# Performance work log

Hardware: AMD Instinct MI355X
Metric: run time of the kernel (lower is better)

## Reference

```python
import jax, jax.numpy as jnp
import numpy as np

A = 256          # image height (x_shape[0])
B = 256          # image width  (x_shape[1])
N = 64           # filterbank grid size
H_DIM = 1024     # hidden dim
BATCH = 512
MAX_DIM = max(A, B)


def _compute_F(params):
    """Build NxA and NxB Gaussian filterbank matrices from 5 attention params.
    Faithful to the torch code: .item() calls on g_X, g_Y, d cut gradients,
    replicated here with stop_gradient; global (not row-wise) normalization;
    var = exp(params[2] + 1e-8) as in the source."""
    gt_X, gt_Y = params[0], params[1]
    var = jnp.exp(params[2] + 1e-8)
    dt = jnp.exp(params[3])
    g_X = jax.lax.stop_gradient((A + 1) * (gt_X + 1) / 2)
    g_Y = jax.lax.stop_gradient((B + 1) * (gt_Y + 1) / 2)
    d = jax.lax.stop_gradient(dt * (MAX_DIM - 1) / (N - 1))
    sub_val = (-N * 0.5 - 0.5) * d  # first linspace endpoint offset; step == d
    idx = jnp.arange(N, dtype=params.dtype)
    mu_X = g_X + sub_val + d * idx  # == linspace(g_X+sub, g_X+add, N)
    mu_Y = g_Y + sub_val + d * idx
    a = jnp.arange(A, dtype=params.dtype)
    b = jnp.arange(B, dtype=params.dtype)
    F_X = jnp.exp(-(a[None, :] - mu_X[:, None]) ** 2 / (2 * var))  # [N, A]
    F_Y = jnp.exp(-(b[None, :] - mu_Y[:, None]) ** 2 / (2 * var))  # [N, B]
    F_X = F_X / jnp.sum(F_X)
    F_Y = F_Y / jnp.sum(F_Y)
    return F_X, F_Y


def setup_inputs() -> dict:
    key = jax.random.key(0)
    k1, k2, k3, k4, k5 = jax.random.split(key, 5)
    x = jax.random.uniform(k1, (BATCH, A * B), dtype=jnp.float32)
    x_hat = jax.random.normal(k2, (BATCH, A * B), dtype=jnp.float32)
    h = jax.random.normal(k3, (BATCH, H_DIM), dtype=jnp.float32)
    # small init scale keeps exp(params) in a sane range
    W_read_w = jax.random.normal(k4, (5, H_DIM), dtype=jnp.float32) * 0.02
    W_read_b = jax.random.normal(k5, (5,), dtype=jnp.float32) * 0.01
    return {"x": x, "x_hat": x_hat, "h": h, "W_read_w": W_read_w, "W_read_b": W_read_b}


def reference(x, x_hat, h, W_read_w, W_read_b):
    # params from the FIRST batch element only, as in the torch code ([0])
    params = (h @ W_read_w.T + W_read_b)[0]  # [5]
    gamma = jnp.exp(params[4])
    F_X, F_Y = _compute_F(params)
    xi = x.reshape(-1, A, B)
    xh = x_hat.reshape(-1, A, B)

    def filt(im):
        # gamma * F_Y @ im @ F_X^T : [x, N, N]
        return gamma * jnp.einsum('na,xab,mb->xnm', F_Y, im, F_X)

    x_filt = filt(xi).reshape(-1, N * N)
    x_hat_filt = filt(xh).reshape(-1, N * N)
    return jnp.concatenate([x_filt, x_hat_filt], axis=1)  # [batch, 2*N^2]
```

## Files before the change

kernel.cpp:

```cpp
#include <hip/hip_runtime.h>
#include <math.h>

#define N_FILT 64
#define IMG_DIM 256
#define IMG_SZ (256*256)
#define HDIM 1024
#define NBATCH 512


__global__ __launch_bounds__(256) void k_prep(
    const float* __restrict__ h, const float* __restrict__ Ww,
    const float* __restrict__ Wb, int* __restrict__ meta,
    float* __restrict__ fyg, float* __restrict__ fxg)
{
  __shared__ float partial[32];
  __shared__ float par_s[8];
  __shared__ float F[N_FILT*IMG_DIM];
  __shared__ int s_lo[64], s_hi[64], s_glo[16], s_ghi[16];
  __shared__ float ssum[4];
  const int t   = threadIdx.x;
  const int side= blockIdx.x;
  const int wv  = t>>6, ln = t&63;
  float* __restrict__ wout = side ? fxg : fyg;

  {
    float4 z = make_float4(0.f,0.f,0.f,0.f);
    float4* p = (float4*)wout;
    #pragma unroll
    for (int k=0;k<16;++k) p[t + 256*k] = z;
  }

  {
    float s0=0.f,s1=0.f,s2=0.f,s3=0.f,s4=0.f;
    for (int k=t;k<HDIM;k+=256){
      const float hv=h[k];
      s0=fmaf(hv,Ww[k        ],s0);
      s1=fmaf(hv,Ww[HDIM+k   ],s1);
      s2=fmaf(hv,Ww[2*HDIM+k ],s2);
      s3=fmaf(hv,Ww[3*HDIM+k ],s3);
      s4=fmaf(hv,Ww[4*HDIM+k ],s4);
    }
    #pragma unroll
    for (int o=32;o>0;o>>=1){
      s0+=__shfl_down(s0,o); s1+=__shfl_down(s1,o); s2+=__shfl_down(s2,o);
      s3+=__shfl_down(s3,o); s4+=__shfl_down(s4,o);
    }
    if (ln==0){ partial[wv*8+0]=s0; partial[wv*8+1]=s1; partial[wv*8+2]=s2;
                partial[wv*8+3]=s3; partial[wv*8+4]=s4; }
  }
  __syncthreads();
  if (t<5) par_s[t]=partial[t]+partial[8+t]+partial[16+t]+partial[24+t]+Wb[t];
  __syncthreads();

  const float var   = expf(par_s[2]+1e-8f);
  const float dt    = expf(par_s[3]);
  const float gamma = expf(par_s[4]);
  const float gC = 0.5f*257.f*(par_s[side?0:1]+1.f);
  const float d  = dt*(255.f/63.f);
  const float sub= -32.5f*d;
  const float inv2v = 1.f/(2.f*var);
  const float w88v  = 88.f*var;

  if (t<64){
    float mu = gC + sub + d*(float)t;
    float astar = fminf(255.f, fmaxf(0.f, rintf(mu)));
    float t0 = (astar-mu)*(astar-mu);
    float r  = sqrtf(t0 + w88v);
    int lo = (int)ceilf(mu-r); int hi = (int)floorf(mu+r)+1;
    lo = lo<0?0:lo; hi = hi>256?256:hi; if (hi<lo) hi=lo;
    s_lo[t]=lo; s_hi[t]=hi;
  }
  __syncthreads();
  if (t<16){
    int lo=256, hi=0;
    #pragma unroll
    for (int k2=0;k2<4;++k2){ lo=min(lo,s_lo[t*4+k2]); hi=max(hi,s_hi[t*4+k2]); }
    if (hi<lo){lo=0;hi=0;}
    if (side==0){ meta[t]=lo; meta[16+t]=hi; }
    else        { lo &= ~3;  meta[32+t]=lo; meta[48+t]=hi; }
    s_glo[t]=lo; s_ghi[t]=hi;
  }
  float sum=0.f;
  #pragma unroll
  for (int k=0;k<64;++k){
    int idx=t+256*k;
    int n=idx>>8, a=idx&255;
    float mu = gC+sub+d*(float)n;
    float dx=(float)a-mu;
    float e=expf(-dx*dx*inv2v);
    F[idx]=e; sum+=e;
  }
  #pragma unroll
  for (int o=32;o>0;o>>=1) sum+=__shfl_down(sum,o);
  if (ln==0) ssum[wv]=sum;
  __syncthreads();
  const float stot = ssum[0]+ssum[1]+ssum[2]+ssum[3];
  const float sc = (side==0 ? gamma : 1.f)/stot;
  #pragma unroll
  for (int k=0;k<64;++k){
    int idx=t+256*k;
    int n=idx>>8, a=idx&255, g=n>>2;
    int lo=s_glo[g], hi=s_ghi[g];
    if (a>=lo && a<hi) wout[(size_t)((g<<10)+((a-lo)<<2)+(n&3))] = F[idx]*sc;
  }
}

__global__ __launch_bounds__(256, 5) void k_main(
    const float* __restrict__ x, const float* __restrict__ xh,
    const int* __restrict__ meta, const float* __restrict__ fyg,
    const float* __restrict__ fxg, float* __restrict__ out)
{
  __shared__ float Tt[16*256];
  const int bid = blockIdx.x;
  const int lg  = ((bid&7)<<9) | (bid>>3);
  const int img = lg>>2, qq = lg&3;
  const int tid = threadIdx.x;
  const int w    = __builtin_amdgcn_readfirstlane(tid>>6);
  const int lane = tid & 63;
  const float* __restrict__ src = (img<NBATCH) ? (x  + (size_t)img*IMG_SZ)
                                               : (xh + (size_t)(img-NBATCH)*IMG_SZ);
  float* __restrict__ dst = ((img<NBATCH) ? (out + (size_t)img*8192)
                                          : (out + (size_t)(img-NBATCH)*8192 + 4096))
                            + qq*1024;

  {
    const int g  = qq*4 + w;
    const int a0 = __builtin_amdgcn_readfirstlane(meta[g]);
    const int nr = __builtin_amdgcn_readfirstlane(meta[16+g]) - a0;
    const int C  = (nr + 7) >> 3;
    const float* rp0 = src + 4*lane;
    const float* wp  = fyg + ((size_t)g<<10);
    float acc[4][4];
    #pragma unroll
    for (int k2=0;k2<4;++k2){acc[k2][0]=0.f;acc[k2][1]=0.f;acc[k2][2]=0.f;acc[k2][3]=0.f;}
    #pragma unroll 1
    for (int c=0; c<C; ++c){
      float4 A[8];
      float wt0[8], wt1[8], wt2[8], wt3[8];
      #pragma unroll
      for (int j=0;j<8;++j){
        int ra = a0 + c*8 + j; ra = ra>255?255:ra;
        A[j] = *(const float4* __restrict__)(rp0 + (ra<<8));
        int rw = c*8 + j; rw = rw>255?255:rw;
        const float* wr = wp + (rw<<2);
        wt0[j]=wr[0]; wt1[j]=wr[1]; wt2[j]=wr[2]; wt3[j]=wr[3];
      }
      __builtin_amdgcn_sched_barrier(0);
      #pragma unroll
      for (int j=0;j<8;++j){
        acc[0][0]=fmaf(wt0[j],A[j].x,acc[0][0]); acc[0][1]=fmaf(wt0[j],A[j].y,acc[0][1]);
        acc[0][2]=fmaf(wt0[j],A[j].z,acc[0][2]); acc[0][3]=fmaf(wt0[j],A[j].w,acc[0][3]);
        acc[1][0]=fmaf(wt1[j],A[j].x,acc[1][0]); acc[1][1]=fmaf(wt1[j],A[j].y,acc[1][1]);
        acc[1][2]=fmaf(wt1[j],A[j].z,acc[1][2]); acc[1][3]=fmaf(wt1[j],A[j].w,acc[1][3]);
        acc[2][0]=fmaf(wt2[j],A[j].x,acc[2][0]); acc[2][1]=fmaf(wt2[j],A[j].y,acc[2][1]);
        acc[2][2]=fmaf(wt2[j],A[j].z,acc[2][2]); acc[2][3]=fmaf(wt2[j],A[j].w,acc[2][3]);
        acc[3][0]=fmaf(wt3[j],A[j].x,acc[3][0]); acc[3][1]=fmaf(wt3[j],A[j].y,acc[3][1]);
        acc[3][2]=fmaf(wt3[j],A[j].z,acc[3][2]); acc[3][3]=fmaf(wt3[j],A[j].w,acc[3][3]);
      }
      __builtin_amdgcn_sched_barrier(0);
    }
    #pragma unroll
    for (int k2=0;k2<4;++k2){
      const int n = w*4 + k2;
      float4 v; v.x=acc[k2][0]; v.y=acc[k2][1]; v.z=acc[k2][2]; v.w=acc[k2][3];
      *(float4*)&Tt[(n<<8) + ((lane ^ n)<<2)] = v;
    }
  }
  __syncthreads();

  const int nl = lane & 15;
  const int cc = lane >> 4;
  const int q  = w*4 + cc;
  const int lo4 = meta[32+q];
  const int hi  = meta[48+q];
  int ngu = (hi - lo4 + 3) >> 2;
  ngu = max(ngu, __shfl_xor(ngu,16));
  ngu = max(ngu, __shfl_xor(ngu,32));
  const int u0  = lo4 >> 2;
  const float* wq = fxg + ((size_t)q<<10);
  float o0=0.f,o1=0.f,o2=0.f,o3=0.f;
  #pragma unroll 1
  for (int it=0; it<ngu; it+=2){
    const int uA = min(u0+it,   63);
    const int uB = min(u0+it+1, 63);
    const float4 tvA = *(const float4*)&Tt[(nl<<8) + ((uA ^ nl)<<2)];
    const float4 tvB = *(const float4*)&Tt[(nl<<8) + ((uB ^ nl)<<2)];
    const float4 a0w = *(const float4*)(wq + it*16);
    const float4 a1w = *(const float4*)(wq + it*16 + 4);
    const float4 a2w = *(const float4*)(wq + it*16 + 8);
    const float4 a3w = *(const float4*)(wq + it*16 + 12);
    const float4 b0w = *(const float4*)(wq + it*16 + 16);
    const float4 b1w = *(const float4*)(wq + it*16 + 20);
    const float4 b2w = *(const float4*)(wq + it*16 + 24);
    const float4 b3w = *(const float4*)(wq + it*16 + 28);
    __builtin_amdgcn_sched_barrier(0);
    o0=fmaf(tvA.x,a0w.x,fmaf(tvA.y,a1w.x,fmaf(tvA.z,a2w.x,fmaf(tvA.w,a3w.x,o0))));
    o1=fmaf(tvA.x,a0w.y,fmaf(tvA.y,a1w.y,fmaf(tvA.z,a2w.y,fmaf(tvA.w,a3w.y,o1))));
    o2=fmaf(tvA.x,a0w.z,fmaf(tvA.y,a1w.z,fmaf(tvA.z,a2w.z,fmaf(tvA.w,a3w.z,o2))));
    o3=fmaf(tvA.x,a0w.w,fmaf(tvA.y,a1w.w,fmaf(tvA.z,a2w.w,fmaf(tvA.w,a3w.w,o3))));
    if (it+1 < ngu){
      o0=fmaf(tvB.x,b0w.x,fmaf(tvB.y,b1w.x,fmaf(tvB.z,b2w.x,fmaf(tvB.w,b3w.x,o0))));
      o1=fmaf(tvB.x,b0w.y,fmaf(tvB.y,b1w.y,fmaf(tvB.z,b2w.y,fmaf(tvB.w,b3w.y,o1))));
      o2=fmaf(tvB.x,b0w.z,fmaf(tvB.y,b1w.z,fmaf(tvB.z,b2w.z,fmaf(tvB.w,b3w.z,o2))));
      o3=fmaf(tvB.x,b0w.w,fmaf(tvB.y,b1w.w,fmaf(tvB.z,b2w.w,fmaf(tvB.w,b3w.w,o3))));
    }
    __builtin_amdgcn_sched_barrier(0);
  }
  __syncthreads();

  {
    const int m0 = q*4;
    Tt[nl*68 + m0 + 0] = o0; Tt[nl*68 + m0 + 1] = o1;
    Tt[nl*68 + m0 + 2] = o2; Tt[nl*68 + m0 + 3] = o3;
  }
  __syncthreads();
  {
    const int f = tid*4;
    const int n = f>>6, m = f&63;
    const float4 v = *(const float4*)&Tt[n*68+m];
    *(float4*)(dst+f) = v;
  }
}

extern "C" void kernel_launch(void* const* d_in, const int* in_sizes, int n_in,
                              void* d_out, int out_size, void* d_ws, size_t ws_size,
                              hipStream_t stream)
{
  const float* x  = (const float*)d_in[0];
  const float* xh = (const float*)d_in[1];
  const float* h  = (const float*)d_in[2];
  const float* Ww = (const float*)d_in[3];
  const float* Wb = (const float*)d_in[4];
  float* out = (float*)d_out;

  int*   meta = (int*)d_ws;
  float* fyg  = (float*)((char*)d_ws + 256);
  float* fxg  = (float*)((char*)d_ws + 256 + 65536);

  k_prep<<<2, 256, 0, stream>>>(h, Ww, Wb, meta, fyg, fxg);
  k_main<<<8*NBATCH, 256, 0, stream>>>(x, xh, meta, fyg, fxg, out);
}
```

Before: 96.63 us.

## Stream image rows into LDS with double-buffered async global_load_lds

```diff
diff --git a/kernel.cpp b/kernel.cpp
--- a/kernel.cpp
+++ b/kernel.cpp
@@ -7,6 +7,13 @@
 #define HDIM 1024
 #define NBATCH 512
 
+
+__device__ __forceinline__ void gl_lds16(const float* g, float* l){
+  __builtin_amdgcn_global_load_lds(
+      (const __attribute__((address_space(1))) unsigned int*)g,
+      (__attribute__((address_space(3))) unsigned int*)l,
+      16, 0, 0);
+}
 
 __global__ __launch_bounds__(256) void k_prep(
     const float* __restrict__ h, const float* __restrict__ Ww,
@@ -110,6 +117,7 @@
     const int* __restrict__ meta, const float* __restrict__ fyg,
     const float* __restrict__ fxg, float* __restrict__ out)
 {
+  __shared__ float CK[4][2][512];
   __shared__ float Tt[16*256];
   const int bid = blockIdx.x;
   const int lg  = ((bid&7)<<9) | (bid>>3);
@@ -126,38 +134,57 @@
   {
     const int g  = qq*4 + w;
     const int a0 = __builtin_amdgcn_readfirstlane(meta[g]);
-    const int nr = __builtin_amdgcn_readfirstlane(meta[16+g]) - a0;
-    const int C  = (nr + 7) >> 3;
-    const float* rp0 = src + 4*lane;
-    const float* wp  = fyg + ((size_t)g<<10);
+    const int a1 = __builtin_amdgcn_readfirstlane(meta[16+g]);
+    const int C  = (a1 > a0) ? ((a1 - a0 + 1) >> 1) : 1;
+    float* const ckw = &CK[w][0][0];
+    const float* const wp   = fyg + ((size_t)g<<10);
+    const float* const srcL = src + (lane<<2);
+
+    gl_lds16(srcL + ((size_t)min(a0,  255)<<8), ckw);
+    gl_lds16(srcL + ((size_t)min(a0+1,255)<<8), ckw + 256);
+
     float acc[4][4];
     #pragma unroll
     for (int k2=0;k2<4;++k2){acc[k2][0]=0.f;acc[k2][1]=0.f;acc[k2][2]=0.f;acc[k2][3]=0.f;}
+
     #pragma unroll 1
     for (int c=0; c<C; ++c){
-      float4 A[8];
-      float wt0[8], wt1[8], wt2[8], wt3[8];
-      #pragma unroll
-      for (int j=0;j<8;++j){
-        int ra = a0 + c*8 + j; ra = ra>255?255:ra;
-        A[j] = *(const float4* __restrict__)(rp0 + (ra<<8));
-        int rw = c*8 + j; rw = rw>255?255:rw;
-        const float* wr = wp + (rw<<2);
-        wt0[j]=wr[0]; wt1[j]=wr[1]; wt2[j]=wr[2]; wt3[j]=wr[3];
+      float* const buf  = ckw + ((c&1)<<9);
+      float* const nbuf = ckw + (((c&1)^1)<<9);
+      asm volatile("s_waitcnt lgkmcnt(0)" ::: "memory");
+      if (c+1 < C){
+        const int a = a0 + 2*(c+1);
+        gl_lds16(srcL + ((size_t)min(a,  255)<<8), nbuf);
+        gl_lds16(srcL + ((size_t)min(a+1,255)<<8), nbuf + 256);
+        asm volatile("s_waitcnt vmcnt(2)" ::: "memory");
+      } else {
+        asm volatile("s_waitcnt vmcnt(0)" ::: "memory");
       }
       __builtin_amdgcn_sched_barrier(0);
-      #pragma unroll
-      for (int j=0;j<8;++j){
-        acc[0][0]=fmaf(wt0[j],A[j].x,acc[0][0]); acc[0][1]=fmaf(wt0[j],A[j].y,acc[0][1]);
-        acc[0][2]=fmaf(wt0[j],A[j].z,acc[0][2]); acc[0][3]=fmaf(wt0[j],A[j].w,acc[0][3]);
-        acc[1][0]=fmaf(wt1[j],A[j].x,acc[1][0]); acc[1][1]=fmaf(wt1[j],A[j].y,acc[1][1]);
-        acc[1][2]=fmaf(wt1[j],A[j].z,acc[1][2]); acc[1][3]=fmaf(wt1[j],A[j].w,acc[1][3]);
-        acc[2][0]=fmaf(wt2[j],A[j].x,acc[2][0]); acc[2][1]=fmaf(wt2[j],A[j].y,acc[2][1]);
-        acc[2][2]=fmaf(wt2[j],A[j].z,acc[2][2]); acc[2][3]=fmaf(wt2[j],A[j].w,acc[2][3]);
-        acc[3][0]=fmaf(wt3[j],A[j].x,acc[3][0]); acc[3][1]=fmaf(wt3[j],A[j].y,acc[3][1]);
-        acc[3][2]=fmaf(wt3[j],A[j].z,acc[3][2]); acc[3][3]=fmaf(wt3[j],A[j].w,acc[3][3]);
-      }
-      __builtin_amdgcn_sched_barrier(0);
+      const float4 tv0 = *(const float4*)&buf[(lane<<2)];
+      const float4 tv1 = *(const float4*)&buf[256 + (lane<<2)];
+      const int rw0 = min(2*c,   255);
+      const int rw1 = min(2*c+1, 255);
+      const float* wr0 = wp + (rw0<<2);
+      const float* wr1 = wp + (rw1<<2);
+      const float w00=wr0[0], w01=wr0[1], w02=wr0[2], w03=wr0[3];
+      const float w10=wr1[0], w11=wr1[1], w12=wr1[2], w13=wr1[3];
+      acc[0][0]=fmaf(w00,tv0.x,acc[0][0]); acc[0][1]=fmaf(w00,tv0.y,acc[0][1]);
+      acc[0][2]=fmaf(w00,tv0.z,acc[0][2]); acc[0][3]=fmaf(w00,tv0.w,acc[0][3]);
+      acc[1][0]=fmaf(w01,tv0.x,acc[1][0]); acc[1][1]=fmaf(w01,tv0.y,acc[1][1]);
+      acc[1][2]=fmaf(w01,tv0.z,acc[1][2]); acc[1][3]=fmaf(w01,tv0.w,acc[1][3]);
+      acc[2][0]=fmaf(w02,tv0.x,acc[2][0]); acc[2][1]=fmaf(w02,tv0.y,acc[2][1]);
+      acc[2][2]=fmaf(w02,tv0.z,acc[2][2]); acc[2][3]=fmaf(w02,tv0.w,acc[2][3]);
+      acc[3][0]=fmaf(w03,tv0.x,acc[3][0]); acc[3][1]=fmaf(w03,tv0.y,acc[3][1]);
+      acc[3][2]=fmaf(w03,tv0.z,acc[3][2]); acc[3][3]=fmaf(w03,tv0.w,acc[3][3]);
+      acc[0][0]=fmaf(w10,tv1.x,acc[0][0]); acc[0][1]=fmaf(w10,tv1.y,acc[0][1]);
+      acc[0][2]=fmaf(w10,tv1.z,acc[0][2]); acc[0][3]=fmaf(w10,tv1.w,acc[0][3]);
+      acc[1][0]=fmaf(w11,tv1.x,acc[1][0]); acc[1][1]=fmaf(w11,tv1.y,acc[1][1]);
+      acc[1][2]=fmaf(w11,tv1.z,acc[1][2]); acc[1][3]=fmaf(w11,tv1.w,acc[1][3]);
+      acc[2][0]=fmaf(w12,tv1.x,acc[2][0]); acc[2][1]=fmaf(w12,tv1.y,acc[2][1]);
+      acc[2][2]=fmaf(w12,tv1.z,acc[2][2]); acc[2][3]=fmaf(w12,tv1.w,acc[2][3]);
+      acc[3][0]=fmaf(w13,tv1.x,acc[3][0]); acc[3][1]=fmaf(w13,tv1.y,acc[3][1]);
+      acc[3][2]=fmaf(w13,tv1.z,acc[3][2]); acc[3][3]=fmaf(w13,tv1.w,acc[3][3]);
     }
     #pragma unroll
     for (int k2=0;k2<4;++k2){
@@ -193,7 +220,6 @@
     const float4 b1w = *(const float4*)(wq + it*16 + 20);
     const float4 b2w = *(const float4*)(wq + it*16 + 24);
     const float4 b3w = *(const float4*)(wq + it*16 + 28);
-    __builtin_amdgcn_sched_barrier(0);
     o0=fmaf(tvA.x,a0w.x,fmaf(tvA.y,a1w.x,fmaf(tvA.z,a2w.x,fmaf(tvA.w,a3w.x,o0))));
     o1=fmaf(tvA.x,a0w.y,fmaf(tvA.y,a1w.y,fmaf(tvA.z,a2w.y,fmaf(tvA.w,a3w.y,o1))));
     o2=fmaf(tvA.x,a0w.z,fmaf(tvA.y,a1w.z,fmaf(tvA.z,a2w.z,fmaf(tvA.w,a3w.z,o2))));
@@ -204,7 +230,6 @@
       o2=fmaf(tvB.x,b0w.z,fmaf(tvB.y,b1w.z,fmaf(tvB.z,b2w.z,fmaf(tvB.w,b3w.z,o2))));
       o3=fmaf(tvB.x,b0w.w,fmaf(tvB.y,b1w.w,fmaf(tvB.z,b2w.w,fmaf(tvB.w,b3w.w,o3))));
     }
-    __builtin_amdgcn_sched_barrier(0);
   }
   __syncthreads();
 
```

Result: slower. 106.1 us (+9.8%).

## Stream image rows into an LDS ring via async global_load_lds prefetch

Applied to the files above, without the earlier changes.

```diff
diff --git a/kernel.cpp b/kernel.cpp
--- a/kernel.cpp
+++ b/kernel.cpp
@@ -7,6 +7,13 @@
 #define HDIM 1024
 #define NBATCH 512
 
+
+__device__ __forceinline__ void gl_lds16(const float* g, float* l){
+  __builtin_amdgcn_global_load_lds(
+      (const __attribute__((address_space(1))) unsigned int*)g,
+      (__attribute__((address_space(3))) unsigned int*)l,
+      16, 0, 0);
+}
 
 __global__ __launch_bounds__(256) void k_prep(
     const float* __restrict__ h, const float* __restrict__ Ww,
@@ -110,7 +117,7 @@
     const int* __restrict__ meta, const float* __restrict__ fyg,
     const float* __restrict__ fxg, float* __restrict__ out)
 {
-  __shared__ float Tt[16*256];
+  __shared__ float POOL[8192];
   const int bid = blockIdx.x;
   const int lg  = ((bid&7)<<9) | (bid>>3);
   const int img = lg>>2, qq = lg&3;
@@ -126,44 +133,44 @@
   {
     const int g  = qq*4 + w;
     const int a0 = __builtin_amdgcn_readfirstlane(meta[g]);
-    const int nr = __builtin_amdgcn_readfirstlane(meta[16+g]) - a0;
-    const int C  = (nr + 7) >> 3;
-    const float* rp0 = src + 4*lane;
-    const float* wp  = fyg + ((size_t)g<<10);
+    const int a1 = __builtin_amdgcn_readfirstlane(meta[16+g]);
+    const int R  = a1 - a0;
+    float* const ckw = &POOL[w<<11];
+    const float* const wp   = fyg + ((size_t)g<<10);
+    const float* const srcL = src + (lane<<2);
+
+    #pragma unroll
+    for (int j=0;j<6;++j)
+      gl_lds16(srcL + ((size_t)min(a0+j,255)<<8), ckw + (j<<8));
+
     float acc[4][4];
     #pragma unroll
     for (int k2=0;k2<4;++k2){acc[k2][0]=0.f;acc[k2][1]=0.f;acc[k2][2]=0.f;acc[k2][3]=0.f;}
+
     #pragma unroll 1
-    for (int c=0; c<C; ++c){
-      float4 A[8];
-      float wt0[8], wt1[8], wt2[8], wt3[8];
-      #pragma unroll
-      for (int j=0;j<8;++j){
-        int ra = a0 + c*8 + j; ra = ra>255?255:ra;
-        A[j] = *(const float4* __restrict__)(rp0 + (ra<<8));
-        int rw = c*8 + j; rw = rw>255?255:rw;
-        const float* wr = wp + (rw<<2);
-        wt0[j]=wr[0]; wt1[j]=wr[1]; wt2[j]=wr[2]; wt3[j]=wr[3];
-      }
+    for (int r=0; r<R; ++r){
+      asm volatile("s_waitcnt vmcnt(5)" ::: "memory");
       __builtin_amdgcn_sched_barrier(0);
-      #pragma unroll
-      for (int j=0;j<8;++j){
-        acc[0][0]=fmaf(wt0[j],A[j].x,acc[0][0]); acc[0][1]=fmaf(wt0[j],A[j].y,acc[0][1]);
-        acc[0][2]=fmaf(wt0[j],A[j].z,acc[0][2]); acc[0][3]=fmaf(wt0[j],A[j].w,acc[0][3]);
-        acc[1][0]=fmaf(wt1[j],A[j].x,acc[1][0]); acc[1][1]=fmaf(wt1[j],A[j].y,acc[1][1]);
-        acc[1][2]=fmaf(wt1[j],A[j].z,acc[1][2]); acc[1][3]=fmaf(wt1[j],A[j].w,acc[1][3]);
-        acc[2][0]=fmaf(wt2[j],A[j].x,acc[2][0]); acc[2][1]=fmaf(wt2[j],A[j].y,acc[2][1]);
-        acc[2][2]=fmaf(wt2[j],A[j].z,acc[2][2]); acc[2][3]=fmaf(wt2[j],A[j].w,acc[2][3]);
-        acc[3][0]=fmaf(wt3[j],A[j].x,acc[3][0]); acc[3][1]=fmaf(wt3[j],A[j].y,acc[3][1]);
-        acc[3][2]=fmaf(wt3[j],A[j].z,acc[3][2]); acc[3][3]=fmaf(wt3[j],A[j].w,acc[3][3]);
-      }
-      __builtin_amdgcn_sched_barrier(0);
-    }
+      gl_lds16(srcL + ((size_t)min(a0+r+6,255)<<8), ckw + (((r+6)&7)<<8));
+      const float4 tv = *(const float4*)&ckw[((r&7)<<8) + (lane<<2)];
+      const float* wr = wp + (r<<2);
+      const float w0=wr[0], w1=wr[1], w2=wr[2], w3=wr[3];
+      acc[0][0]=fmaf(w0,tv.x,acc[0][0]); acc[0][1]=fmaf(w0,tv.y,acc[0][1]);
+      acc[0][2]=fmaf(w0,tv.z,acc[0][2]); acc[0][3]=fmaf(w0,tv.w,acc[0][3]);
+      acc[1][0]=fmaf(w1,tv.x,acc[1][0]); acc[1][1]=fmaf(w1,tv.y,acc[1][1]);
+      acc[1][2]=fmaf(w1,tv.z,acc[1][2]); acc[1][3]=fmaf(w1,tv.w,acc[1][3]);
+      acc[2][0]=fmaf(w2,tv.x,acc[2][0]); acc[2][1]=fmaf(w2,tv.y,acc[2][1]);
+      acc[2][2]=fmaf(w2,tv.z,acc[2][2]); acc[2][3]=fmaf(w2,tv.w,acc[2][3]);
+      acc[3][0]=fmaf(w3,tv.x,acc[3][0]); acc[3][1]=fmaf(w3,tv.y,acc[3][1]);
+      acc[3][2]=fmaf(w3,tv.z,acc[3][2]); acc[3][3]=fmaf(w3,tv.w,acc[3][3]);
+    }
+    asm volatile("s_waitcnt vmcnt(0)" ::: "memory");
+    __syncthreads();
     #pragma unroll
     for (int k2=0;k2<4;++k2){
       const int n = w*4 + k2;
       float4 v; v.x=acc[k2][0]; v.y=acc[k2][1]; v.z=acc[k2][2]; v.w=acc[k2][3];
-      *(float4*)&Tt[(n<<8) + ((lane ^ n)<<2)] = v;
+      *(float4*)&POOL[(n<<8) + ((lane ^ n)<<2)] = v;
     }
   }
   __syncthreads();
@@ -183,8 +190,8 @@
   for (int it=0; it<ngu; it+=2){
     const int uA = min(u0+it,   63);
     const int uB = min(u0+it+1, 63);
-    const float4 tvA = *(const float4*)&Tt[(nl<<8) + ((uA ^ nl)<<2)];
-    const float4 tvB = *(const float4*)&Tt[(nl<<8) + ((uB ^ nl)<<2)];
+    const float4 tvA = *(const float4*)&POOL[(nl<<8) + ((uA ^ nl)<<2)];
+    const float4 tvB = *(const float4*)&POOL[(nl<<8) + ((uB ^ nl)<<2)];
     const float4 a0w = *(const float4*)(wq + it*16);
     const float4 a1w = *(const float4*)(wq + it*16 + 4);
     const float4 a2w = *(const float4*)(wq + it*16 + 8);
@@ -193,7 +200,6 @@
     const float4 b1w = *(const float4*)(wq + it*16 + 20);
     const float4 b2w = *(const float4*)(wq + it*16 + 24);
     const float4 b3w = *(const float4*)(wq + it*16 + 28);
-    __builtin_amdgcn_sched_barrier(0);
     o0=fmaf(tvA.x,a0w.x,fmaf(tvA.y,a1w.x,fmaf(tvA.z,a2w.x,fmaf(tvA.w,a3w.x,o0))));
     o1=fmaf(tvA.x,a0w.y,fmaf(tvA.y,a1w.y,fmaf(tvA.z,a2w.y,fmaf(tvA.w,a3w.y,o1))));
     o2=fmaf(tvA.x,a0w.z,fmaf(tvA.y,a1w.z,fmaf(tvA.z,a2w.z,fmaf(tvA.w,a3w.z,o2))));
@@ -204,20 +210,19 @@
       o2=fmaf(tvB.x,b0w.z,fmaf(tvB.y,b1w.z,fmaf(tvB.z,b2w.z,fmaf(tvB.w,b3w.z,o2))));
       o3=fmaf(tvB.x,b0w.w,fmaf(tvB.y,b1w.w,fmaf(tvB.z,b2w.w,fmaf(tvB.w,b3w.w,o3))));
     }
-    __builtin_amdgcn_sched_barrier(0);
   }
   __syncthreads();
 
   {
     const int m0 = q*4;
-    Tt[nl*68 + m0 + 0] = o0; Tt[nl*68 + m0 + 1] = o1;
-    Tt[nl*68 + m0 + 2] = o2; Tt[nl*68 + m0 + 3] = o3;
+    POOL[nl*68 + m0 + 0] = o0; POOL[nl*68 + m0 + 1] = o1;
+    POOL[nl*68 + m0 + 2] = o2; POOL[nl*68 + m0 + 3] = o3;
   }
   __syncthreads();
   {
     const int f = tid*4;
     const int n = f>>6, m = f&63;
-    const float4 v = *(const float4*)&Tt[n*68+m];
+    const float4 v = *(const float4*)&POOL[n*68+m];
     *(float4*)(dst+f) = v;
   }
 }
```

New measurement: 141.5 us. 1.46x slower.
